# Optimization experiments

Measured on AMD Instinct MI355X. Metric: run time of the kernel, lower is better.

The kernel has to match this reference:

```python
import jax, jax.numpy as jnp
import numpy as np

EPS = 1e-5  # BatchNorm2d default eps


def conv1x1_bn(x, W, gamma, beta, mean, var):
    # 1x1 conv (no bias) + BatchNorm2d in inference form.
    # x: (n, Cin, h, w), W: (Cout, Cin)
    y = jnp.einsum('oc,nchw->nohw', W, x)
    inv = gamma / jnp.sqrt(var + EPS)          # (C,)
    return y * inv[None, :, None, None] + (beta - mean * inv)[None, :, None, None]


def setup_inputs() -> dict:
    key = jax.random.key(0)
    ks = jax.random.split(key, 16)
    B, C, H, W = 8, 256, 128, 128
    sd = 1.0 / np.sqrt(C)
    inp = {
        'x':  jax.random.normal(ks[0], (B, C, H, W), jnp.float32),
        'Wk': jax.random.normal(ks[1], (C, C), jnp.float32) * sd,
        'k_gamma': jax.random.uniform(ks[2], (C,), jnp.float32, 0.5, 1.5),
        'k_beta':  jax.random.normal(ks[3], (C,), jnp.float32) * 0.1,
        'k_mean':  jax.random.normal(ks[4], (C,), jnp.float32) * 0.1,
        'k_var':   jax.random.uniform(ks[5], (C,), jnp.float32, 0.5, 1.5),
        'Wq': jax.random.normal(ks[6], (C, C), jnp.float32) * sd,
        'q_gamma': jax.random.uniform(ks[7], (C,), jnp.float32, 0.5, 1.5),
        'q_beta':  jax.random.normal(ks[8], (C,), jnp.float32) * 0.1,
        'q_mean':  jax.random.normal(ks[9], (C,), jnp.float32) * 0.1,
        'q_var':   jax.random.uniform(ks[10], (C,), jnp.float32, 0.5, 1.5),
        'Wv': jax.random.normal(ks[11], (C, C), jnp.float32) * sd,
        'v_gamma': jax.random.uniform(ks[12], (C,), jnp.float32, 0.5, 1.5),
        'v_beta':  jax.random.normal(ks[13], (C,), jnp.float32) * 0.1,
        'v_mean':  jax.random.normal(ks[14], (C,), jnp.float32) * 0.1,
        'v_var':   jax.random.uniform(ks[15], (C,), jnp.float32, 0.5, 1.5),
    }
    return inp


def reference(x, Wk, k_gamma, k_beta, k_mean, k_var,
              Wq, q_gamma, q_beta, q_mean, q_var,
              Wv, v_gamma, v_beta, v_mean, v_var):
    n, c, h, w = x.shape
    k = conv1x1_bn(x, Wk, k_gamma, k_beta, k_mean, k_var).reshape(n, c, h * w)  # (n,C,S)
    q = conv1x1_bn(x, Wq, q_gamma, q_beta, q_mean, q_var).reshape(n, c, h * w)
    v = conv1x1_bn(x, Wv, v_gamma, v_beta, v_mean, v_var).reshape(n, c, h * w)
    # torch: attention = softmax(q @ k^T, dim=2) -> (n, C, C) channel attention
    attn = jax.nn.softmax(jnp.einsum('ncs,nds->ncd', q, k), axis=-1)
    out = jnp.einsum('ncd,nds->ncs', attn, v).reshape(n, c, h, w)
    return out + x  # res = Identity (in_channels == out_channels)
```

## Files before the change

kernel.cpp:

```cpp
#include <hip/hip_runtime.h>


typedef __bf16 bf16x8 __attribute__((ext_vector_type(8)));
typedef float f32x4 __attribute__((ext_vector_type(4)));
typedef unsigned short us8 __attribute__((ext_vector_type(8)));

#define EPS 1e-5f

__device__ __forceinline__ unsigned short f2bf(float f) {
  unsigned int u = __float_as_uint(f);
  u += 0x7fffu + ((u >> 16) & 1u);
  return (unsigned short)(u >> 16);
}
__device__ __forceinline__ float bf2f(unsigned short h) {
  return __uint_as_float(((unsigned int)h) << 16);
}
__device__ __forceinline__ bf16x8 ld_frag(const unsigned short* p) {
  union { us8 u; bf16x8 b; } x;
  x.u = *(const us8*)p;
  return x.b;
}

#define LDB 72
__global__ __launch_bounds__(512, 2) void kGram(const float* __restrict__ x,
                                                float* __restrict__ Gp,
                                                float* __restrict__ rp,
                                                int chunk) {
  __shared__ __align__(16) unsigned short lh[256 * LDB];
  __shared__ __align__(16) unsigned short ll[256 * LDB];
  const int n = blockIdx.y;
  const int k0 = blockIdx.x * chunk;
  const int nkt = chunk >> 6;
  const int tid = threadIdx.x;
  const float* xn = x + (size_t)n * 4194304;

  f32x4 acc[2][16];
  const f32x4 z4 = {0.f, 0.f, 0.f, 0.f};
#pragma unroll
  for (int i = 0; i < 2; ++i)
#pragma unroll
    for (int j = 0; j < 16; ++j) acc[i][j] = z4;
  float rs[4] = {0.f, 0.f, 0.f, 0.f};

  const int lane = tid & 63, w = tid >> 6;
  const int m = lane & 15, q = lane >> 4;

  for (int kt = 0; kt < nkt; ++kt) {
    const int kb = k0 + kt * 64;
    __syncthreads();
#pragma unroll
    for (int u = 0; u < 4; ++u) {
      const int idx = tid + u * 512;
      const int row = idx >> 3, g = idx & 7;
      const float* p = xn + (size_t)row * 16384 + kb + g * 8;
      const float4 v0 = *(const float4*)p;
      const float4 v1 = *(const float4*)(p + 4);
      float fv[8] = {v0.x, v0.y, v0.z, v0.w, v1.x, v1.y, v1.z, v1.w};
      union { unsigned short s[8]; uint4 v; } H, L;
#pragma unroll
      for (int e = 0; e < 8; ++e) {
        const unsigned short h = f2bf(fv[e]);
        H.s[e] = h;
        L.s[e] = f2bf(fv[e] - bf2f(h));
        rs[u] += fv[e];
      }
      *(uint4*)&lh[row * LDB + g * 8] = H.v;
      *(uint4*)&ll[row * LDB + g * 8] = L.v;
    }
    __syncthreads();
#pragma unroll
    for (int kk = 0; kk < 64; kk += 32) {
      bf16x8 Ah[2], Al[2];
#pragma unroll
      for (int i = 0; i < 2; ++i) {
        const int off = (w * 32 + i * 16 + m) * LDB + kk + q * 8;
        Ah[i] = ld_frag(&lh[off]);
        Al[i] = ld_frag(&ll[off]);
      }
#pragma unroll
      for (int j = 0; j < 16; ++j) {
        const int off = (j * 16 + m) * LDB + kk + q * 8;
        const bf16x8 Bh = ld_frag(&lh[off]);
        const bf16x8 Bl = ld_frag(&ll[off]);
#pragma unroll
        for (int i = 0; i < 2; ++i) {
          acc[i][j] = __builtin_amdgcn_mfma_f32_16x16x32_bf16(Ah[i], Bh, acc[i][j], 0, 0, 0);
          acc[i][j] = __builtin_amdgcn_mfma_f32_16x16x32_bf16(Ah[i], Bl, acc[i][j], 0, 0, 0);
          acc[i][j] = __builtin_amdgcn_mfma_f32_16x16x32_bf16(Al[i], Bh, acc[i][j], 0, 0, 0);
        }
      }
    }
  }
  const size_t slot = (size_t)n * gridDim.x + blockIdx.x;
#pragma unroll
  for (int u = 0; u < 4; ++u) {
    float v = rs[u];
    v += __shfl_xor(v, 1);
    v += __shfl_xor(v, 2);
    v += __shfl_xor(v, 4);
    if ((lane & 7) == 0) rp[slot * 256 + ((tid + u * 512) >> 3)] = v;
  }
  float* Gpn = Gp + slot * 65536;
#pragma unroll
  for (int i = 0; i < 2; ++i)
#pragma unroll
    for (int j = 0; j < 16; ++j)
#pragma unroll
      for (int e = 0; e < 4; ++e) {
        const int grow = w * 32 + i * 16 + q * 4 + e;
        const int gcol = j * 16 + m;
        Gpn[grow * 256 + gcol] = acc[i][j][e];
      }
}

__global__ void kReduce(const float* __restrict__ Gp, float* __restrict__ G,
                        int splits) {
  const int e = blockIdx.x * 256 + threadIdx.x;
  const int n = e >> 16, el = e & 65535;
  const float* p = Gp + (size_t)n * splits * 65536 + el;
  float s = 0.f;
  for (int i = 0; i < splits; ++i) s += p[(size_t)i * 65536];
  G[e] = s;
}

__global__ __launch_bounds__(256) void kAttn(
    const float* __restrict__ G, const float* __restrict__ rp, int splits,
    const float* __restrict__ Wq, const float* __restrict__ qga, const float* __restrict__ qbe,
    const float* __restrict__ qme, const float* __restrict__ qva,
    const float* __restrict__ Wk, const float* __restrict__ kga, const float* __restrict__ kbe,
    const float* __restrict__ kme, const float* __restrict__ kva,
    const float* __restrict__ Wv, const float* __restrict__ vga, const float* __restrict__ vbe,
    const float* __restrict__ vme, const float* __restrict__ vva,
    unsigned short* __restrict__ M, float* __restrict__ cvec) {
  __shared__ float a_lds[16 * 256];
  __shared__ float t_lds[16 * 256];
  __shared__ float r_lds[256];
  __shared__ float iv_lds[256], bv_lds[256];
  __shared__ float rq_lds[16], bq_lds[16], rsum_lds[16];

  const int n = blockIdx.y, r0 = blockIdx.x * 16;
  const int t = threadIdx.x;
  const float* Gn = G + (size_t)n * 65536;

  {
    float s = 0.f;
    const float* p = rp + (size_t)n * splits * 256 + t;
    for (int ss = 0; ss < splits; ++ss) s += p[ss * 256];
    r_lds[t] = s;
  }
  {
    const float iv = vga[t] * rsqrtf(vva[t] + EPS);
    iv_lds[t] = iv;
    bv_lds[t] = vbe[t] - vme[t] * iv;
  }
#pragma unroll
  for (int u = 0; u < 16; ++u) {
    const int idx = t + u * 256;
    const int i = idx >> 8, j = idx & 255;
    const int c = r0 + i;
    const float iv = qga[c] * rsqrtf(qva[c] + EPS);
    a_lds[idx] = iv * Wq[c * 256 + j];
  }
  if (t < 16) {
    const int c = r0 + t;
    const float iv = qga[c] * rsqrtf(qva[c] + EPS);
    bq_lds[t] = qbe[c] - qme[c] * iv;
  }
  __syncthreads();

  if (t < 16) {
    float s = 0.f;
    for (int k2 = 0; k2 < 256; ++k2) s += a_lds[t * 256 + k2] * r_lds[k2];
    rq_lds[t] = s;
  }
  float treg[16];
#pragma unroll
  for (int i = 0; i < 16; ++i) treg[i] = 0.f;
  for (int k2 = 0; k2 < 256; ++k2) {
    const float g = Gn[k2 * 256 + t];
#pragma unroll
    for (int i = 0; i < 16; ++i) treg[i] += a_lds[i * 256 + k2] * g;
  }
#pragma unroll
  for (int i = 0; i < 16; ++i) t_lds[i * 256 + t] = treg[i];
  __syncthreads();

  float lreg[16];
#pragma unroll
  for (int i = 0; i < 16; ++i) lreg[i] = 0.f;
  const float ivk = kga[t] * rsqrtf(kva[t] + EPS);
  const float bkd = kbe[t] - kme[t] * ivk;
  float rkd = 0.f;
  const float* wkrow = Wk + t * 256;
  for (int j = 0; j < 256; j += 4) {
    const float4 w4 = *(const float4*)&wkrow[j];
    const float b0 = ivk * w4.x, b1 = ivk * w4.y, b2 = ivk * w4.z, b3 = ivk * w4.w;
    rkd += b0 * r_lds[j] + b1 * r_lds[j + 1] + b2 * r_lds[j + 2] + b3 * r_lds[j + 3];
#pragma unroll
    for (int i = 0; i < 16; ++i) {
      lreg[i] += t_lds[i * 256 + j] * b0 + t_lds[i * 256 + j + 1] * b1 +
                 t_lds[i * 256 + j + 2] * b2 + t_lds[i * 256 + j + 3] * b3;
    }
  }
  __syncthreads();
#pragma unroll
  for (int i = 0; i < 16; ++i)
    a_lds[i * 256 + t] = lreg[i] + rq_lds[i] * bkd + bq_lds[i] * rkd + 16384.0f * bq_lds[i] * bkd;
  __syncthreads();

  {
    const int i = t >> 4, g = t & 15;
    float* row = a_lds + i * 256;
    float mx = -1e30f;
#pragma unroll
    for (int u = 0; u < 16; ++u) mx = fmaxf(mx, row[g + u * 16]);
    mx = fmaxf(mx, __shfl_xor(mx, 1));
    mx = fmaxf(mx, __shfl_xor(mx, 2));
    mx = fmaxf(mx, __shfl_xor(mx, 4));
    mx = fmaxf(mx, __shfl_xor(mx, 8));
    float sm = 0.f;
#pragma unroll
    for (int u = 0; u < 16; ++u) {
      const int d = g + u * 16;
      const float p = __expf(row[d] - mx);
      row[d] = p;
      sm += p;
    }
    sm += __shfl_xor(sm, 1);
    sm += __shfl_xor(sm, 2);
    sm += __shfl_xor(sm, 4);
    sm += __shfl_xor(sm, 8);
    if (g == 0) rsum_lds[i] = sm;
  }
  __syncthreads();

  float mreg[16];
#pragma unroll
  for (int i = 0; i < 16; ++i) mreg[i] = 0.f;
  for (int d = 0; d < 256; ++d) {
    const float wv = iv_lds[d] * Wv[d * 256 + t];
#pragma unroll
    for (int i = 0; i < 16; ++i) mreg[i] += a_lds[i * 256 + d] * wv;
  }
#pragma unroll
  for (int i = 0; i < 16; ++i) {
    const float inv = 1.0f / rsum_lds[i];
    M[((size_t)n * 256 + r0 + i) * 256 + t] = f2bf(mreg[i] * inv);
  }
  if (t < 16) {
    float cv = 0.f;
    for (int d = 0; d < 256; ++d) cv += a_lds[t * 256 + d] * bv_lds[d];
    cvec[n * 256 + r0 + t] = cv / rsum_lds[t];
  }
}

#define LDT 40
__global__ __launch_bounds__(256, 2) void kOut(const float* __restrict__ x,
                                               const unsigned short* __restrict__ M,
                                               const float* __restrict__ cvec,
                                               float* __restrict__ out) {
  __shared__ __align__(16) unsigned short xt[64 * LDT];
  __shared__ __align__(16) float xf[256 * 64];
  const int n = blockIdx.y, s0 = blockIdx.x * 64;
  const int tid = threadIdx.x;
  const float* xn = x + (size_t)n * 4194304;
  const unsigned short* Mn = M + (size_t)n * 65536;
  const int lane = tid & 63, w = tid >> 6;
  const int m = lane & 15, q = lane >> 4;

  f32x4 acc[4][4];
  const f32x4 z4 = {0.f, 0.f, 0.f, 0.f};
#pragma unroll
  for (int i = 0; i < 4; ++i)
#pragma unroll
    for (int ct = 0; ct < 4; ++ct) acc[i][ct] = z4;

  for (int kt = 0; kt < 8; ++kt) {
    __syncthreads();
#pragma unroll
    for (int u = 0; u < 2; ++u) {
      const int fidx = tid + u * 256;
      const int ch = fidx >> 4, f = fidx & 15;
      const float4 v = *(const float4*)(xn + (size_t)(kt * 32 + ch) * 16384 + s0 + f * 4);
      *(float4*)&xf[(kt * 32 + ch) * 64 + f * 4] = v;
      xt[(f * 4 + 0) * LDT + ch] = f2bf(v.x);
      xt[(f * 4 + 1) * LDT + ch] = f2bf(v.y);
      xt[(f * 4 + 2) * LDT + ch] = f2bf(v.z);
      xt[(f * 4 + 3) * LDT + ch] = f2bf(v.w);
    }
    __syncthreads();
    bf16x8 A[4], B[4];
#pragma unroll
    for (int i = 0; i < 4; ++i)
      A[i] = ld_frag(&Mn[((w * 4 + i) * 16 + m) * 256 + kt * 32 + q * 8]);
#pragma unroll
    for (int ct = 0; ct < 4; ++ct)
      B[ct] = ld_frag(&xt[(ct * 16 + m) * LDT + q * 8]);
#pragma unroll
    for (int i = 0; i < 4; ++i)
#pragma unroll
      for (int ct = 0; ct < 4; ++ct)
        acc[i][ct] = __builtin_amdgcn_mfma_f32_16x16x32_bf16(A[i], B[ct], acc[i][ct], 0, 0, 0);
  }
#pragma unroll
  for (int i = 0; i < 4; ++i) {
    const int cb = w * 64 + i * 16 + q * 4;
#pragma unroll
    for (int e = 0; e < 4; ++e) {
      const int c = cb + e;
      const float cv = cvec[n * 256 + c];
      float* orow = out + ((size_t)n * 256 + c) * 16384 + s0;
#pragma unroll
      for (int ct = 0; ct < 4; ++ct) {
        const int s = ct * 16 + m;
        orow[s] = acc[i][ct][e] + cv + xf[c * 64 + s];
      }
    }
  }
}

extern "C" void kernel_launch(void* const* d_in, const int* in_sizes, int n_in,
                              void* d_out, int out_size, void* d_ws, size_t ws_size,
                              hipStream_t stream) {
  const float* x   = (const float*)d_in[0];
  const float* Wk  = (const float*)d_in[1];
  const float* kga = (const float*)d_in[2];
  const float* kbe = (const float*)d_in[3];
  const float* kme = (const float*)d_in[4];
  const float* kva = (const float*)d_in[5];
  const float* Wq  = (const float*)d_in[6];
  const float* qga = (const float*)d_in[7];
  const float* qbe = (const float*)d_in[8];
  const float* qme = (const float*)d_in[9];
  const float* qva = (const float*)d_in[10];
  const float* Wv  = (const float*)d_in[11];
  const float* vga = (const float*)d_in[12];
  const float* vbe = (const float*)d_in[13];
  const float* vme = (const float*)d_in[14];
  const float* vva = (const float*)d_in[15];

  char* ws = (char*)d_ws;
  float* G           = (float*)(ws);
  unsigned short* Mm = (unsigned short*)(ws + 2097152);
  float* cv          = (float*)(ws + 3145728);
  float* rp          = (float*)(ws + 3153920);
  float* Gp          = (float*)(ws + 3416064);
  float* out         = (float*)d_out;

  int splits = 32;
  while (splits > 1 &&
         (size_t)3416064 + (size_t)splits * 8 * 65536 * 4 > ws_size)
    splits >>= 1;
  const int chunk = 16384 / splits;

  kGram<<<dim3(splits, 8), 512, 0, stream>>>(x, Gp, rp, chunk);
  kReduce<<<2048, 256, 0, stream>>>(Gp, G, splits);
  kAttn<<<dim3(16, 8), 256, 0, stream>>>(G, rp, splits,
                                         Wq, qga, qbe, qme, qva,
                                         Wk, kga, kbe, kme, kva,
                                         Wv, vga, vbe, vme, vva,
                                         Mm, cv);
  kOut<<<dim3(256, 8), 256, 0, stream>>>(x, Mm, cv, out);
}
```

Measured before the change: 417.2 us.

## Vectorize split reduction and restructure attention kernel with more blocks

```diff
diff --git a/kernel.cpp b/kernel.cpp
--- a/kernel.cpp
+++ b/kernel.cpp
@@ -115,14 +115,18 @@
 
 __global__ void kReduce(const float* __restrict__ Gp, float* __restrict__ G,
                         int splits) {
-  const int e = blockIdx.x * 256 + threadIdx.x;
-  const int n = e >> 16, el = e & 65535;
+  const int e4 = (blockIdx.x * 256 + threadIdx.x) * 4;
+  const int n = e4 >> 16, el = e4 & 65535;
   const float* p = Gp + (size_t)n * splits * 65536 + el;
-  float s = 0.f;
-  for (int i = 0; i < splits; ++i) s += p[(size_t)i * 65536];
-  G[e] = s;
-}
-
+  float4 s = {0.f, 0.f, 0.f, 0.f};
+  for (int i = 0; i < splits; ++i) {
+    const float4 v = *(const float4*)(p + (size_t)i * 65536);
+    s.x += v.x; s.y += v.y; s.z += v.z; s.w += v.w;
+  }
+  *(float4*)(G + e4) = s;
+}
+
+#define TLD 260
 __global__ __launch_bounds__(256) void kAttn(
     const float* __restrict__ G, const float* __restrict__ rp, int splits,
     const float* __restrict__ Wq, const float* __restrict__ qga, const float* __restrict__ qbe,
@@ -132,14 +136,16 @@
     const float* __restrict__ Wv, const float* __restrict__ vga, const float* __restrict__ vbe,
     const float* __restrict__ vme, const float* __restrict__ vva,
     unsigned short* __restrict__ M, float* __restrict__ cvec) {
-  __shared__ float a_lds[16 * 256];
-  __shared__ float t_lds[16 * 256];
-  __shared__ float r_lds[256];
-  __shared__ float iv_lds[256], bv_lds[256];
-  __shared__ float rq_lds[16], bq_lds[16], rsum_lds[16];
-
-  const int n = blockIdx.y, r0 = blockIdx.x * 16;
+  __shared__ __align__(16) float t_lds[8 * TLD];
+  __shared__ __align__(16) float p_lds[8 * TLD];
+  __shared__ __align__(16) float r_lds[256];
+  __shared__ float ivv_lds[256], bv_lds[256];
+  __shared__ float rq_lds[8], bq_lds[8], rsum_lds[8];
+
+  const int n = blockIdx.y, r0 = blockIdx.x * 8;
   const int t = threadIdx.x;
+  const int lane = t & 63;
+  const int w = __builtin_amdgcn_readfirstlane(t >> 6);
   const float* Gn = G + (size_t)n * 65536;
 
   {
@@ -147,110 +153,129 @@
     const float* p = rp + (size_t)n * splits * 256 + t;
     for (int ss = 0; ss < splits; ++ss) s += p[ss * 256];
     r_lds[t] = s;
-  }
-  {
     const float iv = vga[t] * rsqrtf(vva[t] + EPS);
-    iv_lds[t] = iv;
+    ivv_lds[t] = iv;
     bv_lds[t] = vbe[t] - vme[t] * iv;
   }
-#pragma unroll
-  for (int u = 0; u < 16; ++u) {
-    const int idx = t + u * 256;
-    const int i = idx >> 8, j = idx & 255;
-    const int c = r0 + i;
-    const float iv = qga[c] * rsqrtf(qva[c] + EPS);
-    a_lds[idx] = iv * Wq[c * 256 + j];
-  }
-  if (t < 16) {
-    const int c = r0 + t;
-    const float iv = qga[c] * rsqrtf(qva[c] + EPS);
-    bq_lds[t] = qbe[c] - qme[c] * iv;
-  }
   __syncthreads();
 
-  if (t < 16) {
-    float s = 0.f;
-    for (int k2 = 0; k2 < 256; ++k2) s += a_lds[t * 256 + k2] * r_lds[k2];
-    rq_lds[t] = s;
-  }
-  float treg[16];
-#pragma unroll
-  for (int i = 0; i < 16; ++i) treg[i] = 0.f;
-  for (int k2 = 0; k2 < 256; ++k2) {
-    const float g = Gn[k2 * 256 + t];
-#pragma unroll
-    for (int i = 0; i < 16; ++i) treg[i] += a_lds[i * 256 + k2] * g;
-  }
-#pragma unroll
-  for (int i = 0; i < 16; ++i) t_lds[i * 256 + t] = treg[i];
+  const int c0 = r0 + 2 * w, c1 = c0 + 1;
+  const float ivq0 = qga[c0] * rsqrtf(qva[c0] + EPS);
+  const float ivq1 = qga[c1] * rsqrtf(qva[c1] + EPS);
+
+  {
+    const float4 r4 = *(const float4*)(r_lds + lane * 4);
+#pragma unroll
+    for (int rr = 0; rr < 2; ++rr) {
+      const float4 w4 = *(const float4*)(Wq + (size_t)(c0 + rr) * 256 + lane * 4);
+      float s = w4.x * r4.x + w4.y * r4.y + w4.z * r4.z + w4.w * r4.w;
+      s += __shfl_xor(s, 1);  s += __shfl_xor(s, 2);  s += __shfl_xor(s, 4);
+      s += __shfl_xor(s, 8);  s += __shfl_xor(s, 16); s += __shfl_xor(s, 32);
+      if (lane == 0) rq_lds[2 * w + rr] = s * (rr ? ivq1 : ivq0);
+    }
+    if (lane == 0) {
+      bq_lds[2 * w + 0] = qbe[c0] - qme[c0] * ivq0;
+      bq_lds[2 * w + 1] = qbe[c1] - qme[c1] * ivq1;
+    }
+  }
+
+  {
+    float4 tr0 = {0.f, 0.f, 0.f, 0.f}, tr1 = {0.f, 0.f, 0.f, 0.f};
+    const float* wq0 = Wq + (size_t)c0 * 256;
+    const float* wq1 = Wq + (size_t)c1 * 256;
+    for (int kb = 0; kb < 256; kb += 4) {
+      union { float4 v; float f[4]; } A0, A1;
+      A0.v = *(const float4*)(wq0 + kb);
+      A1.v = *(const float4*)(wq1 + kb);
+#pragma unroll
+      for (int e = 0; e < 4; ++e) {
+        const float4 g4 = *(const float4*)(Gn + (size_t)(kb + e) * 256 + lane * 4);
+        const float a0 = A0.f[e], a1 = A1.f[e];
+        tr0.x += a0 * g4.x; tr0.y += a0 * g4.y; tr0.z += a0 * g4.z; tr0.w += a0 * g4.w;
+        tr1.x += a1 * g4.x; tr1.y += a1 * g4.y; tr1.z += a1 * g4.z; tr1.w += a1 * g4.w;
+      }
+    }
+    tr0.x *= ivq0; tr0.y *= ivq0; tr0.z *= ivq0; tr0.w *= ivq0;
+    tr1.x *= ivq1; tr1.y *= ivq1; tr1.z *= ivq1; tr1.w *= ivq1;
+    *(float4*)(t_lds + (2 * w + 0) * TLD + lane * 4) = tr0;
+    *(float4*)(t_lds + (2 * w + 1) * TLD + lane * 4) = tr1;
+  }
   __syncthreads();
 
-  float lreg[16];
-#pragma unroll
-  for (int i = 0; i < 16; ++i) lreg[i] = 0.f;
-  const float ivk = kga[t] * rsqrtf(kva[t] + EPS);
-  const float bkd = kbe[t] - kme[t] * ivk;
-  float rkd = 0.f;
-  const float* wkrow = Wk + t * 256;
-  for (int j = 0; j < 256; j += 4) {
-    const float4 w4 = *(const float4*)&wkrow[j];
-    const float b0 = ivk * w4.x, b1 = ivk * w4.y, b2 = ivk * w4.z, b3 = ivk * w4.w;
-    rkd += b0 * r_lds[j] + b1 * r_lds[j + 1] + b2 * r_lds[j + 2] + b3 * r_lds[j + 3];
-#pragma unroll
-    for (int i = 0; i < 16; ++i) {
-      lreg[i] += t_lds[i * 256 + j] * b0 + t_lds[i * 256 + j + 1] * b1 +
-                 t_lds[i * 256 + j + 2] * b2 + t_lds[i * 256 + j + 3] * b3;
-    }
+  {
+    float lreg[8];
+#pragma unroll
+    for (int i = 0; i < 8; ++i) lreg[i] = 0.f;
+    const float ivk = kga[t] * rsqrtf(kva[t] + EPS);
+    const float bkd = kbe[t] - kme[t] * ivk;
+    float rkd = 0.f;
+    const float* wkrow = Wk + (size_t)t * 256;
+    for (int jb = 0; jb < 256; jb += 4) {
+      const float4 w4 = *(const float4*)(wkrow + jb);
+      const float4 r4 = *(const float4*)(r_lds + jb);
+      rkd += w4.x * r4.x + w4.y * r4.y + w4.z * r4.z + w4.w * r4.w;
+#pragma unroll
+      for (int i = 0; i < 8; ++i) {
+        const float4 t4 = *(const float4*)(t_lds + i * TLD + jb);
+        lreg[i] += t4.x * w4.x + t4.y * w4.y + t4.z * w4.z + t4.w * w4.w;
+      }
+    }
+#pragma unroll
+    for (int i = 0; i < 8; ++i)
+      p_lds[i * TLD + t] = ivk * lreg[i] + rq_lds[i] * bkd +
+                           bq_lds[i] * (ivk * rkd) + 16384.0f * bq_lds[i] * bkd;
   }
   __syncthreads();
-#pragma unroll
-  for (int i = 0; i < 16; ++i)
-    a_lds[i * 256 + t] = lreg[i] + rq_lds[i] * bkd + bq_lds[i] * rkd + 16384.0f * bq_lds[i] * bkd;
-  __syncthreads();
-
-  {
-    const int i = t >> 4, g = t & 15;
-    float* row = a_lds + i * 256;
+
+  {
+    const int i = t >> 5, s = t & 31;
+    float* row = p_lds + i * TLD;
     float mx = -1e30f;
 #pragma unroll
-    for (int u = 0; u < 16; ++u) mx = fmaxf(mx, row[g + u * 16]);
+    for (int u = 0; u < 8; ++u) mx = fmaxf(mx, row[s + u * 32]);
     mx = fmaxf(mx, __shfl_xor(mx, 1));
     mx = fmaxf(mx, __shfl_xor(mx, 2));
     mx = fmaxf(mx, __shfl_xor(mx, 4));
     mx = fmaxf(mx, __shfl_xor(mx, 8));
-    float sm = 0.f;
-#pragma unroll
-    for (int u = 0; u < 16; ++u) {
-      const int d = g + u * 16;
-      const float p = __expf(row[d] - mx);
-      row[d] = p;
-      sm += p;
-    }
-    sm += __shfl_xor(sm, 1);
-    sm += __shfl_xor(sm, 2);
-    sm += __shfl_xor(sm, 4);
-    sm += __shfl_xor(sm, 8);
-    if (g == 0) rsum_lds[i] = sm;
+    mx = fmaxf(mx, __shfl_xor(mx, 16));
+    float sraw = 0.f, sbv = 0.f;
+#pragma unroll
+    for (int u = 0; u < 8; ++u) {
+      const int d = s + u * 32;
+      const float e = __expf(row[d] - mx);
+      sraw += e;
+      sbv += e * bv_lds[d];
+      row[d] = e * ivv_lds[d];
+    }
+    sraw += __shfl_xor(sraw, 1);  sbv += __shfl_xor(sbv, 1);
+    sraw += __shfl_xor(sraw, 2);  sbv += __shfl_xor(sbv, 2);
+    sraw += __shfl_xor(sraw, 4);  sbv += __shfl_xor(sbv, 4);
+    sraw += __shfl_xor(sraw, 8);  sbv += __shfl_xor(sbv, 8);
+    sraw += __shfl_xor(sraw, 16); sbv += __shfl_xor(sbv, 16);
+    if (s == 0) {
+      rsum_lds[i] = sraw;
+      cvec[n * 256 + r0 + i] = sbv / sraw;
+    }
   }
   __syncthreads();
 
-  float mreg[16];
-#pragma unroll
-  for (int i = 0; i < 16; ++i) mreg[i] = 0.f;
-  for (int d = 0; d < 256; ++d) {
-    const float wv = iv_lds[d] * Wv[d * 256 + t];
-#pragma unroll
-    for (int i = 0; i < 16; ++i) mreg[i] += a_lds[i * 256 + d] * wv;
-  }
-#pragma unroll
-  for (int i = 0; i < 16; ++i) {
-    const float inv = 1.0f / rsum_lds[i];
-    M[((size_t)n * 256 + r0 + i) * 256 + t] = f2bf(mreg[i] * inv);
-  }
-  if (t < 16) {
-    float cv = 0.f;
-    for (int d = 0; d < 256; ++d) cv += a_lds[t * 256 + d] * bv_lds[d];
-    cvec[n * 256 + r0 + t] = cv / rsum_lds[t];
+  {
+    float mreg[8];
+#pragma unroll
+    for (int i = 0; i < 8; ++i) mreg[i] = 0.f;
+    for (int db = 0; db < 256; db += 4) {
+      float wv[4];
+#pragma unroll
+      for (int e = 0; e < 4; ++e) wv[e] = Wv[(size_t)(db + e) * 256 + t];
+#pragma unroll
+      for (int i = 0; i < 8; ++i) {
+        const float4 p4 = *(const float4*)(p_lds + i * TLD + db);
+        mreg[i] += p4.x * wv[0] + p4.y * wv[1] + p4.z * wv[2] + p4.w * wv[3];
+      }
+    }
+#pragma unroll
+    for (int i = 0; i < 8; ++i)
+      M[((size_t)n * 256 + r0 + i) * 256 + t] = f2bf(mreg[i] / rsum_lds[i]);
   }
 }
 
@@ -354,8 +379,8 @@
   const int chunk = 16384 / splits;
 
   kGram<<<dim3(splits, 8), 512, 0, stream>>>(x, Gp, rp, chunk);
-  kReduce<<<2048, 256, 0, stream>>>(Gp, G, splits);
-  kAttn<<<dim3(16, 8), 256, 0, stream>>>(G, rp, splits,
+  kReduce<<<512, 256, 0, stream>>>(Gp, G, splits);
+  kAttn<<<dim3(32, 8), 256, 0, stream>>>(G, rp, splits,
                                          Wq, qga, qbe, qme, qva,
                                          Wk, kga, kbe, kme, kva,
                                          Wv, vga, vbe, vme, vva,
```

Measured after the change: 390.7 us. 6.4% less time.
